# Performance work log

Hardware: AMD Instinct MI355X
Metric: run time of the kernel (lower is better)

The kernel has to match this reference:

```python
import jax, jax.numpy as jnp
import numpy as np

N_HEAD, D_MODEL, D_K, D_V = 8, 512, 64, 64
LN_EPS = 1e-3


def setup_inputs() -> dict:
    key = jax.random.key(0)
    ks = jax.random.split(key, 9)
    B, L = 4, 2048
    q = jax.random.normal(ks[0], (B, L, D_MODEL), dtype=jnp.float32)
    k = jax.random.normal(ks[1], (B, L, D_MODEL), dtype=jnp.float32)
    v = jax.random.normal(ks[2], (B, L, D_MODEL), dtype=jnp.float32)
    # xavier-normal-ish init for projections
    s_qk = (2.0 / (D_MODEL + D_K)) ** 0.5
    s_v = (2.0 / (D_MODEL + D_V)) ** 0.5
    s_p = (2.0 / (N_HEAD * D_V + D_MODEL)) ** 0.5
    w_qs = jax.random.normal(ks[3], (N_HEAD, D_MODEL, D_K), dtype=jnp.float32) * s_qk
    w_ks = jax.random.normal(ks[4], (N_HEAD, D_MODEL, D_K), dtype=jnp.float32) * s_qk
    w_vs = jax.random.normal(ks[5], (N_HEAD, D_MODEL, D_V), dtype=jnp.float32) * s_v
    proj_w = jax.random.normal(ks[6], (D_MODEL, N_HEAD * D_V), dtype=jnp.float32) * s_p  # torch Linear weight (out,in)
    proj_b = jnp.zeros((D_MODEL,), dtype=jnp.float32)
    a_2 = jnp.ones((D_MODEL,), dtype=jnp.float32)
    b_2 = jnp.zeros((D_MODEL,), dtype=jnp.float32)
    return {"q": q, "k": k, "v": v, "w_qs": w_qs, "w_ks": w_ks, "w_vs": w_vs,
            "proj_w": proj_w, "proj_b": proj_b, "a_2": a_2, "b_2": b_2}


def _layer_norm(z, a_2, b_2):
    # torch.std default is unbiased (ddof=1); module divides by (sigma + eps)
    mu = jnp.mean(z, axis=-1, keepdims=True)
    sigma = jnp.std(z, axis=-1, keepdims=True, ddof=1)
    return (z - mu) / (sigma + LN_EPS) * a_2 + b_2


def reference(q, k, v, w_qs, w_ks, w_vs, proj_w, proj_b, a_2, b_2):
    B, Lq, D = q.shape
    temper = jnp.asarray(D, q.dtype) ** 0.5  # note: sqrt(d_model), as in source
    residual = q
    # per-head projections: (h, b, l, dk)
    qh = jnp.einsum('bld,hdk->hblk', q, w_qs)
    kh = jnp.einsum('bmd,hdk->hbmk', k, w_ks)
    vh = jnp.einsum('bmd,hdv->hbmv', v, w_vs)
    # full score matrix (h, b, lq, lk) -- faithful to naive bmm attention
    attn = jax.nn.softmax(jnp.einsum('hblk,hbmk->hblm', qh, kh) / temper, axis=-1)
    out = jnp.einsum('hblm,hbmv->hblv', attn, vh)          # (h, b, lq, dv)
    out = jnp.transpose(out, (1, 2, 0, 3)).reshape(B, Lq, -1)  # concat heads -> (b, lq, h*dv)
    out = out @ proj_w.T + proj_b
    out = _layer_norm(out + residual, a_2, b_2)
    attns = attn.reshape(-1, attn.shape[2], attn.shape[3])  # (h*b, lq, lk) matching torch layout
    return out, attns
```

## Files before the change

kernel.cpp:

```cpp
#include <hip/hip_runtime.h>
#include <stdint.h>

typedef unsigned short u16;
typedef u16   u16x4v __attribute__((ext_vector_type(4)));
typedef u16   u16x8v __attribute__((ext_vector_type(8)));
typedef short s16x8v __attribute__((ext_vector_type(8)));
typedef float f32x4v __attribute__((ext_vector_type(4)));

#define DEV static __device__ __forceinline__

DEV u16 f2bf(float f){
  union { float f; unsigned u; } v; v.f = f;
  unsigned r = v.u + 0x7FFFu + ((v.u >> 16) & 1u);
  return (u16)(r >> 16);
}

DEV f32x4v mfma16(s16x8v a, s16x8v b, f32x4v c){
  return __builtin_amdgcn_mfma_f32_16x16x32_bf16(a, b, c, 0, 0, 0);
}

__global__ __launch_bounds__(256) void k_wall(const float* __restrict__ w_qs,
                                              const float* __restrict__ w_ks,
                                              const float* __restrict__ w_vs,
                                              const float* __restrict__ proj_w,
                                              u16* __restrict__ wt, u16* __restrict__ wtp,
                                              float qscale){
  int gid = blockIdx.x;
  int tsel = gid >> 10;
  int e = (gid & 1023) * 256 + threadIdx.x;
  if(tsel == 3){
    wtp[e] = f2bf(proj_w[e]);
  } else {
    const float* w = tsel == 0 ? w_qs : (tsel == 1 ? w_ks : w_vs);
    float sc = tsel == 0 ? qscale : 1.0f;
    int n = e >> 9, d = e & 511;
    int h = n >> 6, kk = n & 63;
    wt[tsel * 262144 + n * 512 + d] = f2bf(w[h * 32768 + d * 64 + kk] * sc);
  }
}

__global__ __launch_bounds__(256) void k_qkv(const float* __restrict__ Q,
                                             const float* __restrict__ K,
                                             const float* __restrict__ V,
                                             const u16* __restrict__ Wt,
                                             u16* __restrict__ qhh, u16* __restrict__ khh,
                                             u16* __restrict__ vtt){
  __shared__ __align__(16) u16 Xs[32 * 520];
  const int t = threadIdx.x;
  const int lane = t & 63, w = t >> 6;
  const int g = lane >> 4, li = lane & 15;
  const int i0 = blockIdx.x * 32;
  const int y = blockIdx.y;
  const int tsel = y >> 1;
  const float* X = tsel == 0 ? Q : (tsel == 1 ? K : V);
  const int n0 = (y & 1) * 256 + w * 64;

  #pragma unroll
  for(int it = 0; it < 16; ++it){
    int s = it * 256 + t, row = s >> 7, c4 = s & 127;
    f32x4v xv = *(const f32x4v*)(X + (size_t)(i0 + row) * 512 + c4 * 4);
    u16x4v bv; bv[0]=f2bf(xv[0]); bv[1]=f2bf(xv[1]); bv[2]=f2bf(xv[2]); bv[3]=f2bf(xv[3]);
    *(u16x4v*)(Xs + row * 520 + c4 * 4) = bv;
  }
  __syncthreads();

  const int wbase = tsel * 512 + n0;
  const u16* wp0 = Wt + (size_t)(wbase +  0 + li) * 512 + g * 8;
  const u16* wp1 = Wt + (size_t)(wbase + 16 + li) * 512 + g * 8;
  const u16* wp2 = Wt + (size_t)(wbase + 32 + li) * 512 + g * 8;
  const u16* wp3 = Wt + (size_t)(wbase + 48 + li) * 512 + g * 8;

#define LOADW(S, c) { \
  S##0 = *(const s16x8v*)(wp0 + (c) * 32); \
  S##1 = *(const s16x8v*)(wp1 + (c) * 32); \
  S##2 = *(const s16x8v*)(wp2 + (c) * 32); \
  S##3 = *(const s16x8v*)(wp3 + (c) * 32); }
#define COMPW(S, c) { \
  int k0 = (c) * 32 + g * 8; \
  s16x8v a0 = *(const s16x8v*)(Xs + li * 520 + k0); \
  s16x8v a1 = *(const s16x8v*)(Xs + (16 + li) * 520 + k0); \
  acc[0][0] = mfma16(a0, S##0, acc[0][0]); acc[1][0] = mfma16(a1, S##0, acc[1][0]); \
  acc[0][1] = mfma16(a0, S##1, acc[0][1]); acc[1][1] = mfma16(a1, S##1, acc[1][1]); \
  acc[0][2] = mfma16(a0, S##2, acc[0][2]); acc[1][2] = mfma16(a1, S##2, acc[1][2]); \
  acc[0][3] = mfma16(a0, S##3, acc[0][3]); acc[1][3] = mfma16(a1, S##3, acc[1][3]); }

  f32x4v acc[2][4] = {};
  s16x8v wA0, wA1, wA2, wA3, wB0, wB1, wB2, wB3;
  LOADW(wA, 0);
  #pragma unroll
  for(int c = 0; c < 16; c += 2){
    LOADW(wB, c + 1);
    COMPW(wA, c);
    if(c + 2 < 16) LOADW(wA, c + 2);
    COMPW(wB, c + 1);
  }
#undef LOADW
#undef COMPW

  if(tsel < 2){
    u16* Y = tsel == 0 ? qhh : khh;
    #pragma unroll
    for(int rg = 0; rg < 2; ++rg)
      #pragma unroll
      for(int j = 0; j < 4; ++j){
        int n = n0 + j * 16 + li, h = n >> 6, dk = n & 63;
        #pragma unroll
        for(int r = 0; r < 4; ++r){
          int i = i0 + rg * 16 + g * 4 + r, bb = i >> 11, m = i & 2047;
          Y[((size_t)(h * 4 + bb) * 2048 + m) * 64 + dk] = f2bf(acc[rg][j][r]);
        }
      }
  } else {
    #pragma unroll
    for(int rg = 0; rg < 2; ++rg)
      #pragma unroll
      for(int j = 0; j < 4; ++j){
        int n = n0 + j * 16 + li;
        u16x4v pk;
        #pragma unroll
        for(int r = 0; r < 4; ++r) pk[r] = f2bf(acc[rg][j][r]);
        *(u16x4v*)(vtt + (size_t)n * 8192 + i0 + g * 8 + rg * 4) = pk;
      }
  }
}


#define LOADK(B, ht) { \
  const u16* _p = kp + (size_t)(ht) * 2048; \
  B##0 = *(const s16x8v*)(_p); \
  B##1 = *(const s16x8v*)(_p + 32); \
  B##2 = *(const s16x8v*)(_p + 1024); \
  B##3 = *(const s16x8v*)(_p + 1056); }

#define STEPA(B) { \
  f32x4v z0 = {}, z1 = {}; \
  z0 = mfma16(B##0, bq00, z0); z0 = mfma16(B##1, bq01, z0); \
  z1 = mfma16(B##2, bq00, z1); z1 = mfma16(B##3, bq01, z1); \
  _Pragma("unroll") for(int r = 0; r < 4; ++r){ s00[r] += exp2f(z0[r]); s01[r] += exp2f(z1[r]); } \
  f32x4v y0 = {}, y1 = {}; \
  y0 = mfma16(B##0, bq10, y0); y0 = mfma16(B##1, bq11, y0); \
  y1 = mfma16(B##2, bq10, y1); y1 = mfma16(B##3, bq11, y1); \
  _Pragma("unroll") for(int r = 0; r < 4; ++r){ s10[r] += exp2f(y0[r]); s11[r] += exp2f(y1[r]); } }

#define LOADV(B, ht) { \
  const u16* _p = vp + (ht) * 32; \
  B##0 = *(const s16x8v*)(_p); \
  B##1 = *(const s16x8v*)(_p + 131072); \
  B##2 = *(const s16x8v*)(_p + 262144); \
  B##3 = *(const s16x8v*)(_p + 393216); }

#define QS_HALF(KB, VB, bqa, bqb, lb, qs_, ht) { \
  f32x4v z0 = {}, z1 = {}; \
  z0 = mfma16(KB##0, bqa, z0); z0 = mfma16(KB##1, bqb, z0); \
  z1 = mfma16(KB##2, bqa, z1); z1 = mfma16(KB##3, bqb, z1); \
  f32x4v p0, p1; \
  _Pragma("unroll") for(int r = 0; r < 4; ++r){ p0[r] = exp2f(z0[r] + lb); p1[r] = exp2f(z1[r] + lb); } \
  float* _ab = attb + (size_t)((qs_) * 16 + li) * 2048 + (ht) * 32 + g * 4; \
  *(f32x4v*)(_ab) = p0; \
  *(f32x4v*)(_ab + 16) = p1; \
  union { u16 hh[8]; s16x8v v; } _u; \
  _Pragma("unroll") for(int r = 0; r < 4; ++r){ _u.hh[r] = f2bf(p0[r]); _u.hh[4 + r] = f2bf(p1[r]); } \
  acc##qs_##0 = mfma16(_u.v, VB##0, acc##qs_##0); \
  acc##qs_##1 = mfma16(_u.v, VB##1, acc##qs_##1); \
  acc##qs_##2 = mfma16(_u.v, VB##2, acc##qs_##2); \
  acc##qs_##3 = mfma16(_u.v, VB##3, acc##qs_##3); }

#define STEPB(KB, VB, ht) { \
  QS_HALF(KB, VB, bq00, bq01, lb0, 0, ht); \
  QS_HALF(KB, VB, bq10, bq11, lb1, 1, ht); }

__global__ __launch_bounds__(256, 3) void k_attn(const u16* __restrict__ QHH, const u16* __restrict__ KHH,
                                                 const u16* __restrict__ VTT,
                                                 u16* __restrict__ XC, float* __restrict__ ATT){
  __shared__ float Lp[2][2][32];
  __shared__ float AccS[2][32][64];
  const int t = threadIdx.x, lane = t & 63, w = t >> 6;
  const int g = lane >> 4, li = lane & 15;
  const int qs = w >> 1, mh = w & 1;
  const int gid = blockIdx.x;
  const int xcd = gid & 7, rem = gid >> 3;
  const int qt = rem & 31;
  const int hb = xcd * 4 + (rem >> 5);
  const int h = hb >> 2, b = hb & 3;
  const size_t base_hb = (size_t)hb * 2048;
  const int qbase = qt * 64 + qs * 32;

  s16x8v bq00, bq01, bq10, bq11;
  {
    const u16* qp0 = QHH + (base_hb + qbase + li) * 64 + g * 8;
    const u16* qp1 = QHH + (base_hb + qbase + 16 + li) * 64 + g * 8;
    bq00 = *(const s16x8v*)(qp0); bq01 = *(const s16x8v*)(qp0 + 32);
    bq10 = *(const s16x8v*)(qp1); bq11 = *(const s16x8v*)(qp1 + 32);
  }
  const u16* kp = KHH + (base_hb + li) * 64 + g * 8 + (size_t)mh * 65536;
  const u16* vp = VTT + (size_t)(h * 64 + li) * 8192 + b * 2048 + g * 8 + mh * 1024;
  float* attb = ATT + (base_hb + qbase) * 2048 + mh * 1024;

  f32x4v s00 = {}, s01 = {}, s10 = {}, s11 = {};
  {
    s16x8v kA0, kA1, kA2, kA3, kB0, kB1, kB2, kB3;
    LOADK(kA, 0);
    for(int ht = 0; ht < 30; ht += 2){
      LOADK(kB, ht + 1);
      STEPA(kA);
      LOADK(kA, ht + 2);
      STEPA(kB);
    }
    LOADK(kB, 31);
    STEPA(kA);
    STEPA(kB);
  }
  float l0 = (s00[0]+s00[1]+s00[2]+s00[3]) + (s01[0]+s01[1]+s01[2]+s01[3]);
  float l1 = (s10[0]+s10[1]+s10[2]+s10[3]) + (s11[0]+s11[1]+s11[2]+s11[3]);
  l0 += __shfl_xor(l0, 16, 64); l0 += __shfl_xor(l0, 32, 64);
  l1 += __shfl_xor(l1, 16, 64); l1 += __shfl_xor(l1, 32, 64);
  if(lane < 16){ Lp[qs][mh][li] = l0; Lp[qs][mh][16 + li] = l1; }
  __syncthreads();
  const float lb0 = -__log2f(Lp[qs][0][li]      + Lp[qs][1][li]);
  const float lb1 = -__log2f(Lp[qs][0][16 + li] + Lp[qs][1][16 + li]);

  f32x4v acc00 = {}, acc01 = {}, acc02 = {}, acc03 = {};
  f32x4v acc10 = {}, acc11 = {}, acc12 = {}, acc13 = {};
  {
    s16x8v kA0, kA1, kA2, kA3, kB0, kB1, kB2, kB3;
    s16x8v vA0, vA1, vA2, vA3, vB0, vB1, vB2, vB3;
    LOADK(kA, 0); LOADV(vA, 0);
    for(int ht = 0; ht < 30; ht += 2){
      LOADK(kB, ht + 1); LOADV(vB, ht + 1);
      STEPB(kA, vA, ht);
      LOADK(kA, ht + 2); LOADV(vA, ht + 2);
      STEPB(kB, vB, ht + 1);
    }
    LOADK(kB, 31); LOADV(vB, 31);
    STEPB(kA, vA, 30);
    STEPB(kB, vB, 31);
  }

  if(mh == 1){
    #pragma unroll
    for(int r = 0; r < 4; ++r){
      AccS[qs][ 0 + r][lane] = acc00[r];
      AccS[qs][ 4 + r][lane] = acc01[r];
      AccS[qs][ 8 + r][lane] = acc02[r];
      AccS[qs][12 + r][lane] = acc03[r];
      AccS[qs][16 + r][lane] = acc10[r];
      AccS[qs][20 + r][lane] = acc11[r];
      AccS[qs][24 + r][lane] = acc12[r];
      AccS[qs][28 + r][lane] = acc13[r];
    }
  }
  __syncthreads();
  if(mh == 0){
    #pragma unroll
    for(int r = 0; r < 4; ++r){
      acc00[r] += AccS[qs][ 0 + r][lane];
      acc01[r] += AccS[qs][ 4 + r][lane];
      acc02[r] += AccS[qs][ 8 + r][lane];
      acc03[r] += AccS[qs][12 + r][lane];
      acc10[r] += AccS[qs][16 + r][lane];
      acc11[r] += AccS[qs][20 + r][lane];
      acc12[r] += AccS[qs][24 + r][lane];
      acc13[r] += AccS[qs][28 + r][lane];
    }
    #pragma unroll
    for(int r = 0; r < 4; ++r){
      int row0 = qbase + g * 4 + r;
      int row1 = qbase + 16 + g * 4 + r;
      u16* x0 = XC + (size_t)(b * 2048 + row0) * 512 + h * 64 + li;
      u16* x1 = XC + (size_t)(b * 2048 + row1) * 512 + h * 64 + li;
      x0[0]  = f2bf(acc00[r]); x0[16] = f2bf(acc01[r]); x0[32] = f2bf(acc02[r]); x0[48] = f2bf(acc03[r]);
      x1[0]  = f2bf(acc10[r]); x1[16] = f2bf(acc11[r]); x1[32] = f2bf(acc12[r]); x1[48] = f2bf(acc13[r]);
    }
  }
}

__global__ __launch_bounds__(512) void k_out(const u16* __restrict__ Xb,
                                             const u16* __restrict__ Wtp,
                                             float* __restrict__ Yf,
                                             const float* __restrict__ bias,
                                             const float* __restrict__ resid,
                                             const float* __restrict__ a2,
                                             const float* __restrict__ b2){
  __shared__ __align__(16) u16 Xs[16 * 520];
  __shared__ float sred[8][16], sqred[8][16], muL[16], rsL[16];
  const int t = threadIdx.x;
  const int lane = t & 63, w = t >> 6;
  const int g = lane >> 4, li = lane & 15;
  const int i0 = blockIdx.x * 16;
  const int n0 = w * 64;

  #pragma unroll
  for(int it = 0; it < 2; ++it){
    int s = it * 512 + t, row = s >> 6, c8 = s & 63;
    u16x8v xv = *(const u16x8v*)(Xb + (size_t)(i0 + row) * 512 + c8 * 8);
    *(u16x8v*)(Xs + row * 520 + c8 * 8) = xv;
  }
  __syncthreads();

  const u16* wp0 = Wtp + (size_t)(n0 +  0 + li) * 512 + g * 8;
  const u16* wp1 = Wtp + (size_t)(n0 + 16 + li) * 512 + g * 8;
  const u16* wp2 = Wtp + (size_t)(n0 + 32 + li) * 512 + g * 8;
  const u16* wp3 = Wtp + (size_t)(n0 + 48 + li) * 512 + g * 8;

#define LOADW(S, c) { \
  S##0 = *(const s16x8v*)(wp0 + (c) * 32); \
  S##1 = *(const s16x8v*)(wp1 + (c) * 32); \
  S##2 = *(const s16x8v*)(wp2 + (c) * 32); \
  S##3 = *(const s16x8v*)(wp3 + (c) * 32); }
#define COMPW(S, c) { \
  int k0 = (c) * 32 + g * 8; \
  s16x8v a0 = *(const s16x8v*)(Xs + li * 520 + k0); \
  acc[0] = mfma16(a0, S##0, acc[0]); \
  acc[1] = mfma16(a0, S##1, acc[1]); \
  acc[2] = mfma16(a0, S##2, acc[2]); \
  acc[3] = mfma16(a0, S##3, acc[3]); }

  f32x4v acc[4] = {};
  s16x8v wA0, wA1, wA2, wA3, wB0, wB1, wB2, wB3;
  LOADW(wA, 0);
  #pragma unroll
  for(int c = 0; c < 16; c += 2){
    LOADW(wB, c + 1);
    COMPW(wA, c);
    if(c + 2 < 16) LOADW(wA, c + 2);
    COMPW(wB, c + 1);
  }
#undef LOADW
#undef COMPW

  float zres[4][4];
  #pragma unroll
  for(int j = 0; j < 4; ++j){
    int n = n0 + j * 16 + li;
    float bv = bias[n];
    #pragma unroll
    for(int r = 0; r < 4; ++r){
      int i = i0 + g * 4 + r;
      zres[j][r] = acc[j][r] + bv + resid[(size_t)i * 512 + n];
    }
  }
  #pragma unroll
  for(int r = 0; r < 4; ++r){
    float S = 0.f, SQ = 0.f;
    #pragma unroll
    for(int j = 0; j < 4; ++j){ float zz = zres[j][r]; S += zz; SQ += zz * zz; }
    #pragma unroll
    for(int off = 1; off < 16; off <<= 1){ S += __shfl_xor(S, off, 16); SQ += __shfl_xor(SQ, off, 16); }
    if(li == 0){ sred[w][g * 4 + r] = S; sqred[w][g * 4 + r] = SQ; }
  }
  __syncthreads();
  if(t < 16){
    float S = 0.f, SQ = 0.f;
    #pragma unroll
    for(int ww = 0; ww < 8; ++ww){ S += sred[ww][t]; SQ += sqred[ww][t]; }
    float mu = S * (1.0f / 512.0f);
    float var = (SQ - 512.0f * mu * mu) * (1.0f / 511.0f);
    muL[t] = mu;
    rsL[t] = 1.0f / (sqrtf(fmaxf(var, 0.0f)) + 1e-3f);
  }
  __syncthreads();
  #pragma unroll
  for(int r = 0; r < 4; ++r){
    int rloc = g * 4 + r;
    float mu = muL[rloc], rs = rsL[rloc];
    size_t ib = (size_t)(i0 + rloc) * 512;
    #pragma unroll
    for(int j = 0; j < 4; ++j){
      int n = n0 + j * 16 + li;
      Yf[ib + n] = (zres[j][r] - mu) * rs * a2[n] + b2[n];
    }
  }
}

extern "C" void kernel_launch(void* const* d_in, const int* in_sizes, int n_in,
                              void* d_out, int out_size, void* d_ws, size_t ws_size,
                              hipStream_t stream){
  const float* q      = (const float*)d_in[0];
  const float* k      = (const float*)d_in[1];
  const float* v      = (const float*)d_in[2];
  const float* w_qs   = (const float*)d_in[3];
  const float* w_ks   = (const float*)d_in[4];
  const float* w_vs   = (const float*)d_in[5];
  const float* proj_w = (const float*)d_in[6];
  const float* proj_b = (const float*)d_in[7];
  const float* a2     = (const float*)d_in[8];
  const float* b2     = (const float*)d_in[9];

  char* ws = (char*)d_ws;
  u16* wt    = (u16*)(ws);
  u16* wtp   = (u16*)(ws + 1572864);
  u16* qhh   = (u16*)(ws + 2097152);
  u16* khh   = (u16*)(ws + 10485760);
  u16* vtt   = (u16*)(ws + 18874368);
  u16* xc    = (u16*)(ws + 27262976);

  float* out = (float*)d_out;
  float* att = out + 4194304;

  const float qscale = 0.06375872032774575f;

  k_wall<<<dim3(4096), 256, 0, stream>>>(w_qs, w_ks, w_vs, proj_w, wt, wtp, qscale);
  k_qkv <<<dim3(256, 6), 256, 0, stream>>>(q, k, v, wt, qhh, khh, vtt);
  k_attn<<<dim3(1024), 256, 0, stream>>>(qhh, khh, vtt, xc, att);
  k_out <<<dim3(512), 512, 0, stream>>>(xc, wtp, out, proj_b, q, a2, b2);
}
```

Before: 356.6 us.

## Stage attention probabilities through swizzled LDS for coalesced nontemporal stores

Instead of each lane writing scattered 16-byte fragments of the attention matrix directly from MFMA layout, probabilities are written to a per-wave double-buffered LDS tile with an XOR swizzle. They are then read back in a row-contiguous layout and streamed to global memory with nontemporal stores, one step behind the compute. The aim is to cut the cost of the large fp32 attention write by giving it fuller cache-line coalescing and less cache pollution. In exchange it adds LDS traffic and 32KB of shared memory per block, which may reduce occupancy relative to the 3-blocks launch bound.

Result: faster. 310.4 us (-12.9%).

```diff
diff --git a/kernel.cpp b/kernel.cpp
--- a/kernel.cpp
+++ b/kernel.cpp
@@ -149,15 +149,14 @@
   B##2 = *(const s16x8v*)(_p + 262144); \
   B##3 = *(const s16x8v*)(_p + 393216); }
 
-#define QS_HALF(KB, VB, bqa, bqb, lb, qs_, ht) { \
+#define QSC(KB, VB, bqa, bqb, lb, qs_, PtC) { \
   f32x4v z0 = {}, z1 = {}; \
   z0 = mfma16(KB##0, bqa, z0); z0 = mfma16(KB##1, bqb, z0); \
   z1 = mfma16(KB##2, bqa, z1); z1 = mfma16(KB##3, bqb, z1); \
   f32x4v p0, p1; \
   _Pragma("unroll") for(int r = 0; r < 4; ++r){ p0[r] = exp2f(z0[r] + lb); p1[r] = exp2f(z1[r] + lb); } \
-  float* _ab = attb + (size_t)((qs_) * 16 + li) * 2048 + (ht) * 32 + g * 4; \
-  *(f32x4v*)(_ab) = p0; \
-  *(f32x4v*)(_ab + 16) = p1; \
+  *(f32x4v*)((PtC) + (qs_) * 512 + li * 32 + (((g)     ^ (li & 7)) << 2)) = p0; \
+  *(f32x4v*)((PtC) + (qs_) * 512 + li * 32 + (((g + 4) ^ (li & 7)) << 2)) = p1; \
   union { u16 hh[8]; s16x8v v; } _u; \
   _Pragma("unroll") for(int r = 0; r < 4; ++r){ _u.hh[r] = f2bf(p0[r]); _u.hh[4 + r] = f2bf(p1[r]); } \
   acc##qs_##0 = mfma16(_u.v, VB##0, acc##qs_##0); \
@@ -165,18 +164,31 @@
   acc##qs_##2 = mfma16(_u.v, VB##2, acc##qs_##2); \
   acc##qs_##3 = mfma16(_u.v, VB##3, acc##qs_##3); }
 
-#define STEPB(KB, VB, ht) { \
-  QS_HALF(KB, VB, bq00, bq01, lb0, 0, ht); \
-  QS_HALF(KB, VB, bq10, bq11, lb1, 1, ht); }
+#define CSTEP(KB, VB, PtC) { \
+  QSC(KB, VB, bq00, bq01, lb0, 0, PtC); \
+  QSC(KB, VB, bq10, bq11, lb1, 1, PtC); }
+
+#define QST(PtP, qs_, htp) { \
+  f32x4v q0 = *(const f32x4v*)((PtP) + (qs_) * 512 + rr * 32 + ((cc ^ rr) << 2)); \
+  f32x4v q1 = *(const f32x4v*)((PtP) + (qs_) * 512 + (8 + rr) * 32 + ((cc ^ rr) << 2)); \
+  float* _ab = attb + (size_t)((qs_) * 16 + rr) * 2048 + (htp) * 32 + cc * 4; \
+  __builtin_nontemporal_store(q0, (f32x4v*)(_ab)); \
+  __builtin_nontemporal_store(q1, (f32x4v*)(_ab + 8 * 2048)); }
+
+#define SSTEP(PtP, htp) { QST(PtP, 0, htp); QST(PtP, 1, htp); }
 
 __global__ __launch_bounds__(256, 3) void k_attn(const u16* __restrict__ QHH, const u16* __restrict__ KHH,
                                                  const u16* __restrict__ VTT,
                                                  u16* __restrict__ XC, float* __restrict__ ATT){
   __shared__ float Lp[2][2][32];
   __shared__ float AccS[2][32][64];
+  __shared__ __align__(16) float Pt4[4][2][1024];
   const int t = threadIdx.x, lane = t & 63, w = t >> 6;
   const int g = lane >> 4, li = lane & 15;
+  const int rr = lane >> 3, cc = lane & 7;
   const int qs = w >> 1, mh = w & 1;
+  float* PtA = &Pt4[w][0][0];
+  float* PtB = &Pt4[w][1][0];
   const int gid = blockIdx.x;
   const int xcd = gid & 7, rem = gid >> 3;
   const int qt = rem & 31;
@@ -225,15 +237,19 @@
     s16x8v kA0, kA1, kA2, kA3, kB0, kB1, kB2, kB3;
     s16x8v vA0, vA1, vA2, vA3, vB0, vB1, vB2, vB3;
     LOADK(kA, 0); LOADV(vA, 0);
+    LOADK(kB, 1); LOADV(vB, 1);
+    CSTEP(kA, vA, PtA);
     for(int ht = 0; ht < 30; ht += 2){
-      LOADK(kB, ht + 1); LOADV(vB, ht + 1);
-      STEPB(kA, vA, ht);
       LOADK(kA, ht + 2); LOADV(vA, ht + 2);
-      STEPB(kB, vB, ht + 1);
-    }
-    LOADK(kB, 31); LOADV(vB, 31);
-    STEPB(kA, vA, 30);
-    STEPB(kB, vB, 31);
+      SSTEP(PtA, ht);
+      CSTEP(kB, vB, PtB);
+      LOADK(kB, ht + 3); LOADV(vB, ht + 3);
+      SSTEP(PtB, ht + 1);
+      CSTEP(kA, vA, PtA);
+    }
+    SSTEP(PtA, 30);
+    CSTEP(kB, vB, PtB);
+    SSTEP(PtB, 31);
   }
 
   if(mh == 1){
```

## Offload attention-probability stores to dedicated writer waves via LDS handoff

Applied to the files above, without the earlier changes.

Adds two producer-consumer writer wavefronts to the attention kernel. Compute waves write softmax probability tiles into double-buffered, XOR-swizzled LDS and signal readiness through flags. The writer waves copy each tile to the global attention output with coalesced nontemporal stores. The goal is to take the large attention-matrix global store traffic off the MFMA compute waves. In exchange the block grows to 384 threads, uses more LDS, and depends on spin-wait flag synchronisation that may stall compute waves or lower occupancy.

After: 309.9 us. 1.15x faster.

```diff
diff --git a/kernel.cpp b/kernel.cpp
--- a/kernel.cpp
+++ b/kernel.cpp
@@ -8,6 +8,7 @@
 typedef float f32x4v __attribute__((ext_vector_type(4)));
 
 #define DEV static __device__ __forceinline__
+#define VOLI(x) (*((volatile int*)&(x)))
 
 DEV u16 f2bf(float f){
   union { float f; unsigned u; } v; v.f = f;
@@ -149,15 +150,14 @@
   B##2 = *(const s16x8v*)(_p + 262144); \
   B##3 = *(const s16x8v*)(_p + 393216); }
 
-#define QS_HALF(KB, VB, bqa, bqb, lb, qs_, ht) { \
+#define QSW(KB, VB, bqa, bqb, lb, qs_, tile) { \
   f32x4v z0 = {}, z1 = {}; \
   z0 = mfma16(KB##0, bqa, z0); z0 = mfma16(KB##1, bqb, z0); \
   z1 = mfma16(KB##2, bqa, z1); z1 = mfma16(KB##3, bqb, z1); \
   f32x4v p0, p1; \
   _Pragma("unroll") for(int r = 0; r < 4; ++r){ p0[r] = exp2f(z0[r] + lb); p1[r] = exp2f(z1[r] + lb); } \
-  float* _ab = attb + (size_t)((qs_) * 16 + li) * 2048 + (ht) * 32 + g * 4; \
-  *(f32x4v*)(_ab) = p0; \
-  *(f32x4v*)(_ab + 16) = p1; \
+  *(f32x4v*)((tile) + (qs_) * 512 + li * 32 + (((g)     ^ (li & 7)) << 2)) = p0; \
+  *(f32x4v*)((tile) + (qs_) * 512 + li * 32 + (((g + 4) ^ (li & 7)) << 2)) = p1; \
   union { u16 hh[8]; s16x8v v; } _u; \
   _Pragma("unroll") for(int r = 0; r < 4; ++r){ _u.hh[r] = f2bf(p0[r]); _u.hh[4 + r] = f2bf(p1[r]); } \
   acc##qs_##0 = mfma16(_u.v, VB##0, acc##qs_##0); \
@@ -165,17 +165,25 @@
   acc##qs_##2 = mfma16(_u.v, VB##2, acc##qs_##2); \
   acc##qs_##3 = mfma16(_u.v, VB##3, acc##qs_##3); }
 
-#define STEPB(KB, VB, ht) { \
-  QS_HALF(KB, VB, bq00, bq01, lb0, 0, ht); \
-  QS_HALF(KB, VB, bq10, bq11, lb1, 1, ht); }
-
-__global__ __launch_bounds__(256, 3) void k_attn(const u16* __restrict__ QHH, const u16* __restrict__ KHH,
+#define PSTEP(KB, VB, s) { \
+  if((s) >= 2){ while(VOLI(ackf[w]) < (s) - 2){ __builtin_amdgcn_s_sleep(1); } } \
+  asm volatile("" ::: "memory"); \
+  float* tile = &Ptb[w][(s) & 1][0][0]; \
+  QSW(KB, VB, bq00, bq01, lb0, 0, tile); \
+  QSW(KB, VB, bq10, bq11, lb1, 1, tile); \
+  asm volatile("s_waitcnt lgkmcnt(0)" ::: "memory"); \
+  if(lane == 0) VOLI(rdyf[w]) = (s); }
+
+__global__ __launch_bounds__(384, 3) void k_attn(const u16* __restrict__ QHH, const u16* __restrict__ KHH,
                                                  const u16* __restrict__ VTT,
                                                  u16* __restrict__ XC, float* __restrict__ ATT){
   __shared__ float Lp[2][2][32];
   __shared__ float AccS[2][32][64];
+  __shared__ __align__(16) float Ptb[4][2][2][512];
+  __shared__ int rdyf[4], ackf[4];
   const int t = threadIdx.x, lane = t & 63, w = t >> 6;
   const int g = lane >> 4, li = lane & 15;
+  const int rr = lane >> 3, cc = lane & 7;
   const int qs = w >> 1, mh = w & 1;
   const int gid = blockIdx.x;
   const int xcd = gid & 7, rem = gid >> 3;
@@ -185,72 +193,102 @@
   const size_t base_hb = (size_t)hb * 2048;
   const int qbase = qt * 64 + qs * 32;
 
-  s16x8v bq00, bq01, bq10, bq11;
-  {
+  if(lane == 0){
+    if(w < 4) VOLI(rdyf[w]) = -1;
+    else { VOLI(ackf[(w - 4) * 2]) = -1; VOLI(ackf[(w - 4) * 2 + 1]) = -1; }
+  }
+
+  s16x8v bq00 = {}, bq01 = {}, bq10 = {}, bq11 = {};
+  const u16* kp = nullptr; const u16* vp = nullptr;
+  if(w < 4){
     const u16* qp0 = QHH + (base_hb + qbase + li) * 64 + g * 8;
     const u16* qp1 = QHH + (base_hb + qbase + 16 + li) * 64 + g * 8;
     bq00 = *(const s16x8v*)(qp0); bq01 = *(const s16x8v*)(qp0 + 32);
     bq10 = *(const s16x8v*)(qp1); bq11 = *(const s16x8v*)(qp1 + 32);
-  }
-  const u16* kp = KHH + (base_hb + li) * 64 + g * 8 + (size_t)mh * 65536;
-  const u16* vp = VTT + (size_t)(h * 64 + li) * 8192 + b * 2048 + g * 8 + mh * 1024;
-  float* attb = ATT + (base_hb + qbase) * 2048 + mh * 1024;
-
-  f32x4v s00 = {}, s01 = {}, s10 = {}, s11 = {};
-  {
-    s16x8v kA0, kA1, kA2, kA3, kB0, kB1, kB2, kB3;
-    LOADK(kA, 0);
-    for(int ht = 0; ht < 30; ht += 2){
-      LOADK(kB, ht + 1);
+    kp = KHH + (base_hb + li) * 64 + g * 8 + (size_t)mh * 65536;
+    vp = VTT + (size_t)(h * 64 + li) * 8192 + b * 2048 + g * 8 + mh * 1024;
+
+    f32x4v s00 = {}, s01 = {}, s10 = {}, s11 = {};
+    {
+      s16x8v kA0, kA1, kA2, kA3, kB0, kB1, kB2, kB3;
+      LOADK(kA, 0);
+      for(int ht = 0; ht < 30; ht += 2){
+        LOADK(kB, ht + 1);
+        STEPA(kA);
+        LOADK(kA, ht + 2);
+        STEPA(kB);
+      }
+      LOADK(kB, 31);
       STEPA(kA);
-      LOADK(kA, ht + 2);
       STEPA(kB);
     }
-    LOADK(kB, 31);
-    STEPA(kA);
-    STEPA(kB);
-  }
-  float l0 = (s00[0]+s00[1]+s00[2]+s00[3]) + (s01[0]+s01[1]+s01[2]+s01[3]);
-  float l1 = (s10[0]+s10[1]+s10[2]+s10[3]) + (s11[0]+s11[1]+s11[2]+s11[3]);
-  l0 += __shfl_xor(l0, 16, 64); l0 += __shfl_xor(l0, 32, 64);
-  l1 += __shfl_xor(l1, 16, 64); l1 += __shfl_xor(l1, 32, 64);
-  if(lane < 16){ Lp[qs][mh][li] = l0; Lp[qs][mh][16 + li] = l1; }
-  __syncthreads();
-  const float lb0 = -__log2f(Lp[qs][0][li]      + Lp[qs][1][li]);
-  const float lb1 = -__log2f(Lp[qs][0][16 + li] + Lp[qs][1][16 + li]);
+    float l0 = (s00[0]+s00[1]+s00[2]+s00[3]) + (s01[0]+s01[1]+s01[2]+s01[3]);
+    float l1 = (s10[0]+s10[1]+s10[2]+s10[3]) + (s11[0]+s11[1]+s11[2]+s11[3]);
+    l0 += __shfl_xor(l0, 16, 64); l0 += __shfl_xor(l0, 32, 64);
+    l1 += __shfl_xor(l1, 16, 64); l1 += __shfl_xor(l1, 32, 64);
+    if(lane < 16){ Lp[qs][mh][li] = l0; Lp[qs][mh][16 + li] = l1; }
+  }
+  __syncthreads();
 
   f32x4v acc00 = {}, acc01 = {}, acc02 = {}, acc03 = {};
   f32x4v acc10 = {}, acc11 = {}, acc12 = {}, acc13 = {};
-  {
+
+  if(w < 4){
+    const float lb0 = -__log2f(Lp[qs][0][li]      + Lp[qs][1][li]);
+    const float lb1 = -__log2f(Lp[qs][0][16 + li] + Lp[qs][1][16 + li]);
     s16x8v kA0, kA1, kA2, kA3, kB0, kB1, kB2, kB3;
     s16x8v vA0, vA1, vA2, vA3, vB0, vB1, vB2, vB3;
     LOADK(kA, 0); LOADV(vA, 0);
     for(int ht = 0; ht < 30; ht += 2){
       LOADK(kB, ht + 1); LOADV(vB, ht + 1);
-      STEPB(kA, vA, ht);
+      PSTEP(kA, vA, ht);
       LOADK(kA, ht + 2); LOADV(vA, ht + 2);
-      STEPB(kB, vB, ht + 1);
+      PSTEP(kB, vB, ht + 1);
     }
     LOADK(kB, 31); LOADV(vB, 31);
-    STEPB(kA, vA, 30);
-    STEPB(kB, vB, 31);
-  }
-
-  if(mh == 1){
-    #pragma unroll
-    for(int r = 0; r < 4; ++r){
-      AccS[qs][ 0 + r][lane] = acc00[r];
-      AccS[qs][ 4 + r][lane] = acc01[r];
-      AccS[qs][ 8 + r][lane] = acc02[r];
-      AccS[qs][12 + r][lane] = acc03[r];
-      AccS[qs][16 + r][lane] = acc10[r];
-      AccS[qs][20 + r][lane] = acc11[r];
-      AccS[qs][24 + r][lane] = acc12[r];
-      AccS[qs][28 + r][lane] = acc13[r];
-    }
-  }
-  __syncthreads();
-  if(mh == 0){
+    PSTEP(kA, vA, 30);
+    PSTEP(kB, vB, 31);
+
+    if(mh == 1){
+      #pragma unroll
+      for(int r = 0; r < 4; ++r){
+        AccS[qs][ 0 + r][lane] = acc00[r];
+        AccS[qs][ 4 + r][lane] = acc01[r];
+        AccS[qs][ 8 + r][lane] = acc02[r];
+        AccS[qs][12 + r][lane] = acc03[r];
+        AccS[qs][16 + r][lane] = acc10[r];
+        AccS[qs][20 + r][lane] = acc11[r];
+        AccS[qs][24 + r][lane] = acc12[r];
+        AccS[qs][28 + r][lane] = acc13[r];
+      }
+    }
+  } else {
+    const int cw0 = (w - 4) * 2, cw1 = cw0 + 1;
+    for(int s = 0; s < 32; ++s){
+      #pragma unroll
+      for(int pick = 0; pick < 2; ++pick){
+        const int cwv = pick == 0 ? cw0 : cw1;
+        while(VOLI(rdyf[cwv]) < s){ __builtin_amdgcn_s_sleep(1); }
+        asm volatile("" ::: "memory");
+        const float* tp = &Ptb[cwv][s & 1][0][0];
+        f32x4v q00 = *(const f32x4v*)(tp + rr * 32 + ((cc ^ rr) << 2));
+        f32x4v q01 = *(const f32x4v*)(tp + (8 + rr) * 32 + ((cc ^ rr) << 2));
+        f32x4v q10 = *(const f32x4v*)(tp + 512 + rr * 32 + ((cc ^ rr) << 2));
+        f32x4v q11 = *(const f32x4v*)(tp + 512 + (8 + rr) * 32 + ((cc ^ rr) << 2));
+        asm volatile("s_waitcnt lgkmcnt(0)" ::: "memory");
+        if(lane == 0) VOLI(ackf[cwv]) = s;
+        float* ab = ATT + (base_hb + qt * 64 + (cwv >> 1) * 32 + rr) * 2048
+                        + (cwv & 1) * 1024 + s * 32 + cc * 4;
+        __builtin_nontemporal_store(q00, (f32x4v*)(ab));
+        __builtin_nontemporal_store(q01, (f32x4v*)(ab + 8 * 2048));
+        __builtin_nontemporal_store(q10, (f32x4v*)(ab + 16 * 2048));
+        __builtin_nontemporal_store(q11, (f32x4v*)(ab + 24 * 2048));
+      }
+    }
+  }
+  __syncthreads();
+
+  if(w < 4 && mh == 0){
     #pragma unroll
     for(int r = 0; r < 4; ++r){
       acc00[r] += AccS[qs][ 0 + r][lane];
@@ -401,6 +439,6 @@
 
   k_wall<<<dim3(4096), 256, 0, stream>>>(w_qs, w_ks, w_vs, proj_w, wt, wtp, qscale);
   k_qkv <<<dim3(256, 6), 256, 0, stream>>>(q, k, v, wt, qhh, khh, vtt);
-  k_attn<<<dim3(1024), 256, 0, stream>>>(qhh, khh, vtt, xc, att);
+  k_attn<<<dim3(1024), 384, 0, stream>>>(qhh, khh, vtt, xc, att);
   k_out <<<dim3(512), 512, 0, stream>>>(xc, wtp, out, proj_b, q, a2, b2);
 }
```
